# Performance work log

Hardware: AMD Instinct MI355X
Metric: run time of the kernel (lower is better)

Reference implementation:

```python
import jax, jax.numpy as jnp
import numpy as np

N_NODES = 50000
N_EDGES = 800000
IN_DIM = 1280
HID = 512
EMB = 64
LN_EPS = 1e-5
NEG_SLOPE = 0.2  # DGL GATConv default leaky_relu slope


def setup_inputs() -> dict:
    key = jax.random.key(0)
    ks = jax.random.split(key, 10)
    features = jax.random.normal(ks[0], (N_NODES, IN_DIM), dtype=jnp.float32)
    src = jax.random.randint(ks[1], (N_EDGES,), 0, N_NODES)
    dst = jax.random.randint(ks[2], (N_EDGES,), 0, N_NODES)
    # MLPBlock params: Linear(IN_DIM -> HID) + LayerNorm(HID)
    W1 = jax.random.normal(ks[3], (IN_DIM, HID), dtype=jnp.float32) / np.sqrt(IN_DIM)
    b1 = jnp.zeros((HID,), dtype=jnp.float32)
    ln_g = jnp.ones((HID,), dtype=jnp.float32)
    ln_b = jnp.zeros((HID,), dtype=jnp.float32)
    # GATConv params (num_heads=1): fc (no bias), attn_l, attn_r, output bias
    Wg = jax.random.normal(ks[4], (HID, EMB), dtype=jnp.float32) / np.sqrt(HID)
    attn_l = jax.random.normal(ks[5], (EMB,), dtype=jnp.float32) * 0.1
    attn_r = jax.random.normal(ks[6], (EMB,), dtype=jnp.float32) * 0.1
    bias_g = jnp.zeros((EMB,), dtype=jnp.float32)
    return {"features": features, "src": src, "dst": dst, "W1": W1, "b1": b1,
            "ln_g": ln_g, "ln_b": ln_b, "Wg": Wg, "attn_l": attn_l,
            "attn_r": attn_r, "bias_g": bias_g}


def reference(features, src, dst, W1, b1, ln_g, ln_b, Wg, attn_l, attn_r, bias_g):
    # MLPBlock: linear -> ReLU -> LayerNorm (dropout is identity in eval)
    x = jax.nn.relu(features @ W1 + b1)                     # [N, HID]
    mu = jnp.mean(x, axis=-1, keepdims=True)
    var = jnp.mean(jnp.square(x - mu), axis=-1, keepdims=True)
    x = (x - mu) * jax.lax.rsqrt(var + LN_EPS) * ln_g + ln_b

    # GATConv (single head)
    feat = x @ Wg                                           # [N, EMB]
    el = feat @ attn_l                                      # [N]
    er = feat @ attn_r                                      # [N]
    e = jax.nn.leaky_relu(el[src] + er[dst], NEG_SLOPE)     # [E]

    # edge softmax over incoming edges of each dst node
    m = jax.ops.segment_max(e, dst, num_segments=N_NODES)   # [N]
    ex = jnp.exp(e - m[dst])                                # [E]
    s = jax.ops.segment_sum(ex, dst, num_segments=N_NODES)  # [N]
    a = ex / s[dst]                                         # [E]

    # scatter-aggregate weighted source features
    out = jax.ops.segment_sum(a[:, None] * feat[src], dst, num_segments=N_NODES)
    return out + bias_g                                     # [N, EMB] (head dim squeezed)
```

## Files before the change

### kernel.cpp

```cpp
#include <hip/hip_runtime.h>
#include <hip/hip_bf16.h>
#include <stdint.h>

#define N_NODES 50000
#define N_EDGES 800000
#define IN_DIM 1280
#define HID 512
#define EMB 64
#define M_PAD 50048
#define MT1 391
#define LN_EPS 1e-5f

typedef __attribute__((ext_vector_type(8))) __bf16 bf16x8;
typedef __attribute__((ext_vector_type(4))) float floatx4;

#define AS1C(p) ((const __attribute__((address_space(1))) void*)(p))
#define AS3(p)  ((__attribute__((address_space(3))) void*)(p))

__device__ __forceinline__ unsigned f2bf(float f) {
  unsigned u = __float_as_uint(f);
  u += 0x7FFFu + ((u >> 16) & 1u);
  return u >> 16;
}
__device__ __forceinline__ float bf2f(unsigned short s) {
  return __uint_as_float(((unsigned)s) << 16);
}

__global__ __launch_bounds__(256) void k_prep(const float* __restrict__ W1,
                                              const float* __restrict__ Wg,
                                              unsigned short* __restrict__ B1t,
                                              unsigned short* __restrict__ Wgt,
                                              int* __restrict__ deg) {
  int idx = blockIdx.x * 256 + threadIdx.x;
  if (idx < HID * IN_DIM) {
    int n = idx / IN_DIM;
    int k = idx - n * IN_DIM;
    B1t[idx] = (unsigned short)f2bf(W1[(size_t)k * HID + n]);
  }
  if (idx < EMB * HID) {
    int n = idx >> 9;
    int k = idx & 511;
    Wgt[idx] = (unsigned short)f2bf(Wg[(size_t)k * EMB + n]);
  }
  if (idx < N_NODES) deg[idx] = 0;
}

__global__ __launch_bounds__(256) void k_conv(const float* __restrict__ F,
                                              unsigned short* __restrict__ Fb) {
  size_t base = ((size_t)blockIdx.x * 256 + threadIdx.x) * 8;
  uint4 o;
  if (base < (size_t)N_NODES * IN_DIM) {
    float4 f0 = *(const float4*)(F + base);
    float4 f1 = *(const float4*)(F + base + 4);
    o.x = f2bf(f0.x) | (f2bf(f0.y) << 16);
    o.y = f2bf(f0.z) | (f2bf(f0.w) << 16);
    o.z = f2bf(f1.x) | (f2bf(f1.y) << 16);
    o.w = f2bf(f1.z) | (f2bf(f1.w) << 16);
  } else {
    o = make_uint4(0u, 0u, 0u, 0u);
  }
  *(uint4*)(Fb + base) = o;
}

__device__ __forceinline__ int swz(int r) { return (r ^ (r >> 2)) & 3; }

__global__ __launch_bounds__(256) void k_gemm1(const unsigned short* __restrict__ Abf,
                                               const unsigned short* __restrict__ Bt,
                                               const float* __restrict__ bias1,
                                               unsigned short* __restrict__ xn) {
  __shared__ unsigned short As[128 * 32];
  __shared__ unsigned short Bs[128 * 32];
  const int t = threadIdx.x;
  const int bm = blockIdx.x, bn = blockIdx.y;
  const int w = t >> 6, lane = t & 63, quad = lane >> 4, lr = lane & 15;
  const int wm = (w & 1) * 64, wn = (w >> 1) * 64;

  floatx4 acc[4][4];
#pragma unroll
  for (int i = 0; i < 4; ++i)
#pragma unroll
    for (int j = 0; j < 4; ++j) acc[i][j] = (floatx4){0.f, 0.f, 0.f, 0.f};

  const int r0 = t >> 2, c0 = (t & 3) ^ swz(t >> 2);
  const int r1 = 64 + (t >> 2), c1 = (t & 3) ^ swz(64 + (t >> 2));
  const unsigned short* a0 = Abf + (size_t)(bm * 128 + r0) * IN_DIM + c0 * 8;
  const unsigned short* a1 = Abf + (size_t)(bm * 128 + r1) * IN_DIM + c1 * 8;
  const unsigned short* b0 = Bt + (size_t)(bn * 128 + r0) * IN_DIM + c0 * 8;
  const unsigned short* b1 = Bt + (size_t)(bn * 128 + r1) * IN_DIM + c1 * 8;
  unsigned short* asw = As + w * 512;
  unsigned short* bsw = Bs + w * 512;

  const int q2 = quad ^ swz(lr);

  for (int k0 = 0; k0 < IN_DIM; k0 += 32) {
    __builtin_amdgcn_global_load_lds(AS1C(a0 + k0), AS3(asw), 16, 0, 0);
    __builtin_amdgcn_global_load_lds(AS1C(a1 + k0), AS3(asw + 2048), 16, 0, 0);
    __builtin_amdgcn_global_load_lds(AS1C(b0 + k0), AS3(bsw), 16, 0, 0);
    __builtin_amdgcn_global_load_lds(AS1C(b1 + k0), AS3(bsw + 2048), 16, 0, 0);
    __syncthreads();

    bf16x8 af[4], bfv[4];
#pragma unroll
    for (int mi = 0; mi < 4; ++mi)
      af[mi] = *(const bf16x8*)&As[(wm + mi * 16 + lr) * 32 + q2 * 8];
#pragma unroll
    for (int ni = 0; ni < 4; ++ni)
      bfv[ni] = *(const bf16x8*)&Bs[(wn + ni * 16 + lr) * 32 + q2 * 8];
#pragma unroll
    for (int mi = 0; mi < 4; ++mi)
#pragma unroll
      for (int ni = 0; ni < 4; ++ni)
        acc[mi][ni] = __builtin_amdgcn_mfma_f32_16x16x32_bf16(af[mi], bfv[ni], acc[mi][ni], 0, 0, 0);
    __syncthreads();
  }

#pragma unroll
  for (int mi = 0; mi < 4; ++mi) {
    int gr = bm * 128 + wm + mi * 16 + quad * 4;
#pragma unroll
    for (int ni = 0; ni < 4; ++ni) {
      int gc = bn * 128 + wn + ni * 16 + lr;
      float bv = bias1[gc];
#pragma unroll
      for (int r = 0; r < 4; ++r) {
        float v = acc[mi][ni][r] + bv;
        v = v > 0.f ? v : 0.f;
        xn[(size_t)(gr + r) * HID + gc] = (unsigned short)f2bf(v);
      }
    }
  }
}

__global__ __launch_bounds__(256) void k_ln(unsigned short* __restrict__ xn,
                                            const float* __restrict__ g,
                                            const float* __restrict__ b) {
  int w = threadIdx.x >> 6, lane = threadIdx.x & 63;
  int row = blockIdx.x * 4 + w;
  unsigned short* p = xn + (size_t)row * HID + lane * 8;
  uint4 raw = *(const uint4*)p;
  float x[8];
  x[0] = bf2f((unsigned short)(raw.x & 0xFFFF)); x[1] = bf2f((unsigned short)(raw.x >> 16));
  x[2] = bf2f((unsigned short)(raw.y & 0xFFFF)); x[3] = bf2f((unsigned short)(raw.y >> 16));
  x[4] = bf2f((unsigned short)(raw.z & 0xFFFF)); x[5] = bf2f((unsigned short)(raw.z >> 16));
  x[6] = bf2f((unsigned short)(raw.w & 0xFFFF)); x[7] = bf2f((unsigned short)(raw.w >> 16));
  float s1 = 0.f, s2 = 0.f;
#pragma unroll
  for (int j = 0; j < 8; ++j) { s1 += x[j]; s2 += x[j] * x[j]; }
#pragma unroll
  for (int m = 1; m < 64; m <<= 1) {
    s1 += __shfl_xor(s1, m, 64);
    s2 += __shfl_xor(s2, m, 64);
  }
  float mu = s1 * (1.f / HID);
  float var = s2 * (1.f / HID) - mu * mu;
  float rs = rsqrtf(var + LN_EPS);
  const float* gp = g + lane * 8;
  const float* bp = b + lane * 8;
  float4 g0 = *(const float4*)gp, g1 = *(const float4*)(gp + 4);
  float4 b0 = *(const float4*)bp, b1v = *(const float4*)(bp + 4);
  float y0 = (x[0] - mu) * rs * g0.x + b0.x;
  float y1 = (x[1] - mu) * rs * g0.y + b0.y;
  float y2 = (x[2] - mu) * rs * g0.z + b0.z;
  float y3 = (x[3] - mu) * rs * g0.w + b0.w;
  float y4 = (x[4] - mu) * rs * g1.x + b1v.x;
  float y5 = (x[5] - mu) * rs * g1.y + b1v.y;
  float y6 = (x[6] - mu) * rs * g1.z + b1v.z;
  float y7 = (x[7] - mu) * rs * g1.w + b1v.w;
  uint4 o;
  o.x = f2bf(y0) | (f2bf(y1) << 16);
  o.y = f2bf(y2) | (f2bf(y3) << 16);
  o.z = f2bf(y4) | (f2bf(y5) << 16);
  o.w = f2bf(y6) | (f2bf(y7) << 16);
  *(uint4*)p = o;
}

__global__ __launch_bounds__(256) void k_gemm2(const unsigned short* __restrict__ Xn,
                                               const unsigned short* __restrict__ Wgt,
                                               const float* __restrict__ al,
                                               const float* __restrict__ ar,
                                               float* __restrict__ feat,
                                               float* __restrict__ el,
                                               float* __restrict__ er) {
  __shared__ unsigned short As[128 * 32];
  __shared__ unsigned short Bs[64 * 32];
  const int t = threadIdx.x;
  const int bm = blockIdx.x;
  const int w = t >> 6, lane = t & 63, quad = lane >> 4, lr = lane & 15;

  floatx4 acc[2][4];
#pragma unroll
  for (int i = 0; i < 2; ++i)
#pragma unroll
    for (int j = 0; j < 4; ++j) acc[i][j] = (floatx4){0.f, 0.f, 0.f, 0.f};

  const int r0 = t >> 2, c0 = (t & 3) ^ swz(t >> 2);
  const int r1 = 64 + (t >> 2), c1 = (t & 3) ^ swz(64 + (t >> 2));
  const unsigned short* a0 = Xn + (size_t)(bm * 128 + r0) * HID + c0 * 8;
  const unsigned short* a1 = Xn + (size_t)(bm * 128 + r1) * HID + c1 * 8;
  const unsigned short* b0 = Wgt + (size_t)r0 * HID + c0 * 8;
  unsigned short* asw = As + w * 512;
  unsigned short* bsw = Bs + w * 512;

  const int q2 = quad ^ swz(lr);

  for (int k0 = 0; k0 < HID; k0 += 32) {
    __builtin_amdgcn_global_load_lds(AS1C(a0 + k0), AS3(asw), 16, 0, 0);
    __builtin_amdgcn_global_load_lds(AS1C(a1 + k0), AS3(asw + 2048), 16, 0, 0);
    __builtin_amdgcn_global_load_lds(AS1C(b0 + k0), AS3(bsw), 16, 0, 0);
    __syncthreads();

    bf16x8 af[2], bfv[4];
#pragma unroll
    for (int mi = 0; mi < 2; ++mi)
      af[mi] = *(const bf16x8*)&As[(w * 32 + mi * 16 + lr) * 32 + q2 * 8];
#pragma unroll
    for (int ni = 0; ni < 4; ++ni)
      bfv[ni] = *(const bf16x8*)&Bs[(ni * 16 + lr) * 32 + q2 * 8];
#pragma unroll
    for (int mi = 0; mi < 2; ++mi)
#pragma unroll
      for (int ni = 0; ni < 4; ++ni)
        acc[mi][ni] = __builtin_amdgcn_mfma_f32_16x16x32_bf16(af[mi], bfv[ni], acc[mi][ni], 0, 0, 0);
    __syncthreads();
  }

  float alv[4], arv[4];
#pragma unroll
  for (int ni = 0; ni < 4; ++ni) {
    alv[ni] = al[ni * 16 + lr];
    arv[ni] = ar[ni * 16 + lr];
  }
#pragma unroll
  for (int mi = 0; mi < 2; ++mi) {
    int gr = bm * 128 + w * 32 + mi * 16 + quad * 4;
#pragma unroll
    for (int r = 0; r < 4; ++r) {
      float sl = 0.f, sr2 = 0.f;
#pragma unroll
      for (int ni = 0; ni < 4; ++ni) {
        float v = acc[mi][ni][r];
        feat[(size_t)(gr + r) * EMB + ni * 16 + lr] = v;
        sl += v * alv[ni];
        sr2 += v * arv[ni];
      }
#pragma unroll
      for (int m = 1; m < 16; m <<= 1) {
        sl += __shfl_xor(sl, m, 64);
        sr2 += __shfl_xor(sr2, m, 64);
      }
      if (lr == 0) {
        el[gr + r] = sl;
        er[gr + r] = sr2;
      }
    }
  }
}

__global__ __launch_bounds__(256) void k_hist(const int* __restrict__ dst,
                                              int* __restrict__ deg) {
  int t = blockIdx.x * 256 + threadIdx.x;
  if (t < N_EDGES) atomicAdd(&deg[dst[t]], 1);
}

__global__ __launch_bounds__(256) void k_scan1(const int* __restrict__ deg,
                                               int* __restrict__ rowstart,
                                               int* __restrict__ bsum) {
  __shared__ int sh[256];
  int t = threadIdx.x, i = blockIdx.x * 256 + t;
  int x = (i < N_NODES) ? deg[i] : 0;
  sh[t] = x;
  __syncthreads();
  for (int off = 1; off < 256; off <<= 1) {
    int v = (t >= off) ? sh[t - off] : 0;
    __syncthreads();
    sh[t] += v;
    __syncthreads();
  }
  if (i < N_NODES) rowstart[i] = sh[t] - x;
  if (t == 255) bsum[blockIdx.x] = sh[255];
}

__global__ __launch_bounds__(256) void k_scan2(const int* __restrict__ bsum,
                                               int* __restrict__ boff) {
  __shared__ int sh[256];
  int t = threadIdx.x;
  int x = (t < 196) ? bsum[t] : 0;
  sh[t] = x;
  __syncthreads();
  for (int off = 1; off < 256; off <<= 1) {
    int v = (t >= off) ? sh[t - off] : 0;
    __syncthreads();
    sh[t] += v;
    __syncthreads();
  }
  boff[t] = sh[t] - x;
}

__global__ __launch_bounds__(256) void k_scan3(int* __restrict__ rowstart,
                                               const int* __restrict__ boff,
                                               int* __restrict__ cursor) {
  int i = blockIdx.x * 256 + threadIdx.x;
  if (i < N_NODES) {
    int rs = rowstart[i] + boff[i >> 8];
    rowstart[i] = rs;
    cursor[i] = rs;
  }
}

__global__ __launch_bounds__(256) void k_fill(const int* __restrict__ src,
                                              const int* __restrict__ dst,
                                              int* __restrict__ cursor,
                                              int* __restrict__ csr_src) {
  int t = blockIdx.x * 256 + threadIdx.x;
  if (t >= N_EDGES) return;
  int pos = atomicAdd(&cursor[dst[t]], 1);
  csr_src[pos] = src[t];
}

__global__ __launch_bounds__(256) void k_gat(const int* __restrict__ rowstart,
                                             const int* __restrict__ deg,
                                             const int* __restrict__ csr_src,
                                             const float* __restrict__ el,
                                             const float* __restrict__ er,
                                             const float* __restrict__ feat,
                                             const float* __restrict__ bias_g,
                                             float* __restrict__ out) {
  int w = threadIdx.x >> 6, lane = threadIdx.x & 63;
  int v = blockIdx.x * 4 + w;
  int start = rowstart[v], d = deg[v];
  float erv = er[v];
  float m = -3.4e38f, s = 0.f, O = 0.f;
  for (int i = 0; i < d; ++i) {
    int sv = csr_src[start + i];
    float f = feat[(size_t)sv * EMB + lane];
    float e = el[sv] + erv;
    e = e > 0.f ? e : 0.2f * e;
    if (e <= m) {
      float p = __expf(e - m);
      s += p;
      O = fmaf(p, f, O);
    } else {
      float a = __expf(m - e);
      s = fmaf(s, a, 1.f);
      O = fmaf(O, a, f);
      m = e;
    }
  }
  out[(size_t)v * EMB + lane] = (d > 0 ? O / s : 0.f) + bias_g[lane];
}

extern "C" void kernel_launch(void* const* d_in, const int* in_sizes, int n_in,
                              void* d_out, int out_size, void* d_ws, size_t ws_size,
                              hipStream_t stream) {
  const float* features = (const float*)d_in[0];
  const int* src        = (const int*)d_in[1];
  const int* dst        = (const int*)d_in[2];
  const float* W1       = (const float*)d_in[3];
  const float* b1       = (const float*)d_in[4];
  const float* ln_g     = (const float*)d_in[5];
  const float* ln_b     = (const float*)d_in[6];
  const float* Wg       = (const float*)d_in[7];
  const float* attn_l   = (const float*)d_in[8];
  const float* attn_r   = (const float*)d_in[9];
  const float* bias_g   = (const float*)d_in[10];
  float* out = (float*)d_out;

  char* ws = (char*)d_ws;
  size_t off = 0;
  auto alloc = [&](size_t bytes) {
    char* p = ws + off;
    off = (off + bytes + 255) & ~(size_t)255;
    return p;
  };
  unsigned short* B1t   = (unsigned short*)alloc((size_t)HID * IN_DIM * 2);
  unsigned short* Wgt   = (unsigned short*)alloc((size_t)EMB * HID * 2);
  unsigned short* featbf= (unsigned short*)alloc((size_t)M_PAD * IN_DIM * 2);
  unsigned short* xn    = (unsigned short*)alloc((size_t)M_PAD * HID * 2);
  float* feat           = (float*)alloc((size_t)M_PAD * EMB * 4);
  float* el             = (float*)alloc((size_t)M_PAD * 4);
  float* er             = (float*)alloc((size_t)M_PAD * 4);
  int* deg              = (int*)alloc((size_t)N_NODES * 4);
  int* rowstart         = (int*)alloc((size_t)N_NODES * 4);
  int* cursor           = (int*)alloc((size_t)N_NODES * 4);
  int* bsum             = (int*)alloc(256 * 4);
  int* boff             = (int*)alloc(256 * 4);
  int* csr_src          = (int*)alloc((size_t)N_EDGES * 4);
  (void)ws_size; (void)in_sizes; (void)n_in; (void)out_size;

  k_prep<<<dim3(2560), dim3(256), 0, stream>>>(W1, Wg, B1t, Wgt, deg);
  k_conv<<<dim3(31280), dim3(256), 0, stream>>>(features, featbf);
  k_hist<<<dim3(3125), dim3(256), 0, stream>>>(dst, deg);
  k_scan1<<<dim3(196), dim3(256), 0, stream>>>(deg, rowstart, bsum);
  k_scan2<<<dim3(1), dim3(256), 0, stream>>>(bsum, boff);
  k_scan3<<<dim3(196), dim3(256), 0, stream>>>(rowstart, boff, cursor);
  k_fill<<<dim3(3125), dim3(256), 0, stream>>>(src, dst, cursor, csr_src);
  k_gemm1<<<dim3(MT1, 4), dim3(256), 0, stream>>>(featbf, B1t, b1, xn);
  k_ln<<<dim3(M_PAD / 4), dim3(256), 0, stream>>>(xn, ln_g, ln_b);
  k_gemm2<<<dim3(MT1), dim3(256), 0, stream>>>(xn, Wgt, attn_l, attn_r, feat, el, er);
  k_gat<<<dim3(12500), dim3(256), 0, stream>>>(rowstart, deg, csr_src, el, er, feat, bias_g, out);
}
```

Measured before the change: 701.9 us.

## Fold LayerNorm into GEMM epilogues, fuse conv/hist and scans, widen GEMM1 K-tile

```diff
diff --git a/kernel.cpp b/kernel.cpp
--- a/kernel.cpp
+++ b/kernel.cpp
@@ -28,9 +28,15 @@
 
 __global__ __launch_bounds__(256) void k_prep(const float* __restrict__ W1,
                                               const float* __restrict__ Wg,
+                                              const float* __restrict__ ln_g,
+                                              const float* __restrict__ ln_b,
                                               unsigned short* __restrict__ B1t,
-                                              unsigned short* __restrict__ Wgt,
-                                              int* __restrict__ deg) {
+                                              unsigned short* __restrict__ Wgp,
+                                              float* __restrict__ uvec,
+                                              float* __restrict__ vvec,
+                                              int* __restrict__ deg,
+                                              float* __restrict__ s1,
+                                              float* __restrict__ s2) {
   int idx = blockIdx.x * 256 + threadIdx.x;
   if (idx < HID * IN_DIM) {
     int n = idx / IN_DIM;
@@ -40,36 +46,54 @@
   if (idx < EMB * HID) {
     int n = idx >> 9;
     int k = idx & 511;
-    Wgt[idx] = (unsigned short)f2bf(Wg[(size_t)k * EMB + n]);
+    Wgp[idx] = (unsigned short)f2bf(ln_g[k] * Wg[(size_t)k * EMB + n]);
+  }
+  if (idx < EMB) {
+    float su = 0.f, sv = 0.f;
+    for (int k = 0; k < HID; ++k) {
+      float wv = Wg[(size_t)k * EMB + idx];
+      su += ln_b[k] * wv;
+      sv += ln_g[k] * wv;
+    }
+    uvec[idx] = su;
+    vvec[idx] = sv;
   }
   if (idx < N_NODES) deg[idx] = 0;
-}
-
-__global__ __launch_bounds__(256) void k_conv(const float* __restrict__ F,
-                                              unsigned short* __restrict__ Fb) {
-  size_t base = ((size_t)blockIdx.x * 256 + threadIdx.x) * 8;
-  uint4 o;
-  if (base < (size_t)N_NODES * IN_DIM) {
-    float4 f0 = *(const float4*)(F + base);
-    float4 f1 = *(const float4*)(F + base + 4);
-    o.x = f2bf(f0.x) | (f2bf(f0.y) << 16);
-    o.y = f2bf(f0.z) | (f2bf(f0.w) << 16);
-    o.z = f2bf(f1.x) | (f2bf(f1.y) << 16);
-    o.w = f2bf(f1.z) | (f2bf(f1.w) << 16);
+  if (idx < M_PAD) { s1[idx] = 0.f; s2[idx] = 0.f; }
+}
+
+__global__ __launch_bounds__(256) void k_convhist(const float* __restrict__ F,
+                                                  unsigned short* __restrict__ Fb,
+                                                  const int* __restrict__ dst,
+                                                  int* __restrict__ deg) {
+  if (blockIdx.x < 31280) {
+    size_t base = ((size_t)blockIdx.x * 256 + threadIdx.x) * 8;
+    uint4 o;
+    if (base < (size_t)N_NODES * IN_DIM) {
+      float4 f0 = *(const float4*)(F + base);
+      float4 f1 = *(const float4*)(F + base + 4);
+      o.x = f2bf(f0.x) | (f2bf(f0.y) << 16);
+      o.y = f2bf(f0.z) | (f2bf(f0.w) << 16);
+      o.z = f2bf(f1.x) | (f2bf(f1.y) << 16);
+      o.w = f2bf(f1.z) | (f2bf(f1.w) << 16);
+    } else {
+      o = make_uint4(0u, 0u, 0u, 0u);
+    }
+    *(uint4*)(Fb + base) = o;
   } else {
-    o = make_uint4(0u, 0u, 0u, 0u);
-  }
-  *(uint4*)(Fb + base) = o;
-}
-
-__device__ __forceinline__ int swz(int r) { return (r ^ (r >> 2)) & 3; }
+    int t = (blockIdx.x - 31280) * 256 + threadIdx.x;
+    if (t < N_EDGES) atomicAdd(&deg[dst[t]], 1);
+  }
+}
 
 __global__ __launch_bounds__(256) void k_gemm1(const unsigned short* __restrict__ Abf,
                                                const unsigned short* __restrict__ Bt,
                                                const float* __restrict__ bias1,
-                                               unsigned short* __restrict__ xn) {
-  __shared__ unsigned short As[128 * 32];
-  __shared__ unsigned short Bs[128 * 32];
+                                               unsigned short* __restrict__ xn,
+                                               float* __restrict__ s1,
+                                               float* __restrict__ s2) {
+  __shared__ unsigned short As[128 * 64];
+  __shared__ unsigned short Bs[128 * 64];
   const int t = threadIdx.x;
   const int bm = blockIdx.x, bn = blockIdx.y;
   const int w = t >> 6, lane = t & 63, quad = lane >> 4, lr = lane & 15;
@@ -81,36 +105,44 @@
 #pragma unroll
     for (int j = 0; j < 4; ++j) acc[i][j] = (floatx4){0.f, 0.f, 0.f, 0.f};
 
-  const int r0 = t >> 2, c0 = (t & 3) ^ swz(t >> 2);
-  const int r1 = 64 + (t >> 2), c1 = (t & 3) ^ swz(64 + (t >> 2));
-  const unsigned short* a0 = Abf + (size_t)(bm * 128 + r0) * IN_DIM + c0 * 8;
-  const unsigned short* a1 = Abf + (size_t)(bm * 128 + r1) * IN_DIM + c1 * 8;
-  const unsigned short* b0 = Bt + (size_t)(bn * 128 + r0) * IN_DIM + c0 * 8;
-  const unsigned short* b1 = Bt + (size_t)(bn * 128 + r1) * IN_DIM + c1 * 8;
+  const int rr = t >> 3;
+  const int cc = (t & 7) ^ (rr & 7);
+  const unsigned short* aP[4];
+  const unsigned short* bP[4];
+#pragma unroll
+  for (int j = 0; j < 4; ++j) {
+    aP[j] = Abf + (size_t)(bm * 128 + j * 32 + rr) * IN_DIM + cc * 8;
+    bP[j] = Bt + (size_t)(bn * 128 + j * 32 + rr) * IN_DIM + cc * 8;
+  }
   unsigned short* asw = As + w * 512;
   unsigned short* bsw = Bs + w * 512;
 
-  const int q2 = quad ^ swz(lr);
-
-  for (int k0 = 0; k0 < IN_DIM; k0 += 32) {
-    __builtin_amdgcn_global_load_lds(AS1C(a0 + k0), AS3(asw), 16, 0, 0);
-    __builtin_amdgcn_global_load_lds(AS1C(a1 + k0), AS3(asw + 2048), 16, 0, 0);
-    __builtin_amdgcn_global_load_lds(AS1C(b0 + k0), AS3(bsw), 16, 0, 0);
-    __builtin_amdgcn_global_load_lds(AS1C(b1 + k0), AS3(bsw + 2048), 16, 0, 0);
-    __syncthreads();
-
-    bf16x8 af[4], bfv[4];
-#pragma unroll
-    for (int mi = 0; mi < 4; ++mi)
-      af[mi] = *(const bf16x8*)&As[(wm + mi * 16 + lr) * 32 + q2 * 8];
-#pragma unroll
-    for (int ni = 0; ni < 4; ++ni)
-      bfv[ni] = *(const bf16x8*)&Bs[(wn + ni * 16 + lr) * 32 + q2 * 8];
-#pragma unroll
-    for (int mi = 0; mi < 4; ++mi)
+  const int l7 = lr & 7;
+
+  for (int k0 = 0; k0 < IN_DIM; k0 += 64) {
+#pragma unroll
+    for (int j = 0; j < 4; ++j) {
+      __builtin_amdgcn_global_load_lds(AS1C(aP[j] + k0), AS3(asw + j * 2048), 16, 0, 0);
+      __builtin_amdgcn_global_load_lds(AS1C(bP[j] + k0), AS3(bsw + j * 2048), 16, 0, 0);
+    }
+    __syncthreads();
+
+#pragma unroll
+    for (int h = 0; h < 2; ++h) {
+      const int col = ((h * 4 + quad) ^ l7) * 8;
+      bf16x8 af[4], bfv[4];
+#pragma unroll
+      for (int mi = 0; mi < 4; ++mi)
+        af[mi] = *(const bf16x8*)&As[(wm + mi * 16 + lr) * 64 + col];
 #pragma unroll
       for (int ni = 0; ni < 4; ++ni)
-        acc[mi][ni] = __builtin_amdgcn_mfma_f32_16x16x32_bf16(af[mi], bfv[ni], acc[mi][ni], 0, 0, 0);
+        bfv[ni] = *(const bf16x8*)&Bs[(wn + ni * 16 + lr) * 64 + col];
+#pragma unroll
+      for (int mi = 0; mi < 4; ++mi)
+#pragma unroll
+        for (int ni = 0; ni < 4; ++ni)
+          acc[mi][ni] = __builtin_amdgcn_mfma_f32_16x16x32_bf16(af[mi], bfv[ni], acc[mi][ni], 0, 0, 0);
+    }
     __syncthreads();
   }
 
@@ -118,64 +150,40 @@
   for (int mi = 0; mi < 4; ++mi) {
     int gr = bm * 128 + wm + mi * 16 + quad * 4;
 #pragma unroll
-    for (int ni = 0; ni < 4; ++ni) {
-      int gc = bn * 128 + wn + ni * 16 + lr;
-      float bv = bias1[gc];
-#pragma unroll
-      for (int r = 0; r < 4; ++r) {
-        float v = acc[mi][ni][r] + bv;
+    for (int r = 0; r < 4; ++r) {
+      float ps1 = 0.f, ps2 = 0.f;
+#pragma unroll
+      for (int ni = 0; ni < 4; ++ni) {
+        int gc = bn * 128 + wn + ni * 16 + lr;
+        float v = acc[mi][ni][r] + bias1[gc];
         v = v > 0.f ? v : 0.f;
-        xn[(size_t)(gr + r) * HID + gc] = (unsigned short)f2bf(v);
-      }
-    }
-  }
-}
-
-__global__ __launch_bounds__(256) void k_ln(unsigned short* __restrict__ xn,
-                                            const float* __restrict__ g,
-                                            const float* __restrict__ b) {
-  int w = threadIdx.x >> 6, lane = threadIdx.x & 63;
-  int row = blockIdx.x * 4 + w;
-  unsigned short* p = xn + (size_t)row * HID + lane * 8;
-  uint4 raw = *(const uint4*)p;
-  float x[8];
-  x[0] = bf2f((unsigned short)(raw.x & 0xFFFF)); x[1] = bf2f((unsigned short)(raw.x >> 16));
-  x[2] = bf2f((unsigned short)(raw.y & 0xFFFF)); x[3] = bf2f((unsigned short)(raw.y >> 16));
-  x[4] = bf2f((unsigned short)(raw.z & 0xFFFF)); x[5] = bf2f((unsigned short)(raw.z >> 16));
-  x[6] = bf2f((unsigned short)(raw.w & 0xFFFF)); x[7] = bf2f((unsigned short)(raw.w >> 16));
-  float s1 = 0.f, s2 = 0.f;
-#pragma unroll
-  for (int j = 0; j < 8; ++j) { s1 += x[j]; s2 += x[j] * x[j]; }
-#pragma unroll
-  for (int m = 1; m < 64; m <<= 1) {
-    s1 += __shfl_xor(s1, m, 64);
-    s2 += __shfl_xor(s2, m, 64);
-  }
-  float mu = s1 * (1.f / HID);
-  float var = s2 * (1.f / HID) - mu * mu;
-  float rs = rsqrtf(var + LN_EPS);
-  const float* gp = g + lane * 8;
-  const float* bp = b + lane * 8;
-  float4 g0 = *(const float4*)gp, g1 = *(const float4*)(gp + 4);
-  float4 b0 = *(const float4*)bp, b1v = *(const float4*)(bp + 4);
-  float y0 = (x[0] - mu) * rs * g0.x + b0.x;
-  float y1 = (x[1] - mu) * rs * g0.y + b0.y;
-  float y2 = (x[2] - mu) * rs * g0.z + b0.z;
-  float y3 = (x[3] - mu) * rs * g0.w + b0.w;
-  float y4 = (x[4] - mu) * rs * g1.x + b1v.x;
-  float y5 = (x[5] - mu) * rs * g1.y + b1v.y;
-  float y6 = (x[6] - mu) * rs * g1.z + b1v.z;
-  float y7 = (x[7] - mu) * rs * g1.w + b1v.w;
-  uint4 o;
-  o.x = f2bf(y0) | (f2bf(y1) << 16);
-  o.y = f2bf(y2) | (f2bf(y3) << 16);
-  o.z = f2bf(y4) | (f2bf(y5) << 16);
-  o.w = f2bf(y6) | (f2bf(y7) << 16);
-  *(uint4*)p = o;
-}
+        unsigned short h = (unsigned short)f2bf(v);
+        xn[(size_t)(gr + r) * HID + gc] = h;
+        float vr = bf2f(h);
+        ps1 += vr;
+        ps2 += vr * vr;
+      }
+#pragma unroll
+      for (int m = 1; m < 16; m <<= 1) {
+        ps1 += __shfl_xor(ps1, m, 64);
+        ps2 += __shfl_xor(ps2, m, 64);
+      }
+      if (lr == 0) {
+        atomicAdd(&s1[gr + r], ps1);
+        atomicAdd(&s2[gr + r], ps2);
+      }
+    }
+  }
+}
+
+__device__ __forceinline__ int swz(int r) { return (r ^ (r >> 2)) & 3; }
 
 __global__ __launch_bounds__(256) void k_gemm2(const unsigned short* __restrict__ Xn,
-                                               const unsigned short* __restrict__ Wgt,
+                                               const unsigned short* __restrict__ Wgp,
+                                               const float* __restrict__ s1,
+                                               const float* __restrict__ s2,
+                                               const float* __restrict__ uvec,
+                                               const float* __restrict__ vvec,
                                                const float* __restrict__ al,
                                                const float* __restrict__ ar,
                                                float* __restrict__ feat,
@@ -197,7 +205,7 @@
   const int r1 = 64 + (t >> 2), c1 = (t & 3) ^ swz(64 + (t >> 2));
   const unsigned short* a0 = Xn + (size_t)(bm * 128 + r0) * HID + c0 * 8;
   const unsigned short* a1 = Xn + (size_t)(bm * 128 + r1) * HID + c1 * 8;
-  const unsigned short* b0 = Wgt + (size_t)r0 * HID + c0 * 8;
+  const unsigned short* b0 = Wgp + (size_t)r0 * HID + c0 * 8;
   unsigned short* asw = As + w * 512;
   unsigned short* bsw = Bs + w * 512;
 
@@ -224,22 +232,28 @@
     __syncthreads();
   }
 
-  float alv[4], arv[4];
+  float alv[4], arv[4], uv[4], vv[4];
 #pragma unroll
   for (int ni = 0; ni < 4; ++ni) {
     alv[ni] = al[ni * 16 + lr];
     arv[ni] = ar[ni * 16 + lr];
+    uv[ni] = uvec[ni * 16 + lr];
+    vv[ni] = vvec[ni * 16 + lr];
   }
 #pragma unroll
   for (int mi = 0; mi < 2; ++mi) {
     int gr = bm * 128 + w * 32 + mi * 16 + quad * 4;
 #pragma unroll
     for (int r = 0; r < 4; ++r) {
+      int row = gr + r;
+      float mu = s1[row] * (1.f / HID);
+      float rs = rsqrtf(s2[row] * (1.f / HID) - mu * mu + LN_EPS);
+      float mrs = mu * rs;
       float sl = 0.f, sr2 = 0.f;
 #pragma unroll
       for (int ni = 0; ni < 4; ++ni) {
-        float v = acc[mi][ni][r];
-        feat[(size_t)(gr + r) * EMB + ni * 16 + lr] = v;
+        float v = rs * acc[mi][ni][r] + uv[ni] - mrs * vv[ni];
+        feat[(size_t)row * EMB + ni * 16 + lr] = v;
         sl += v * alv[ni];
         sr2 += v * arv[ni];
       }
@@ -249,17 +263,11 @@
         sr2 += __shfl_xor(sr2, m, 64);
       }
       if (lr == 0) {
-        el[gr + r] = sl;
-        er[gr + r] = sr2;
-      }
-    }
-  }
-}
-
-__global__ __launch_bounds__(256) void k_hist(const int* __restrict__ dst,
-                                              int* __restrict__ deg) {
-  int t = blockIdx.x * 256 + threadIdx.x;
-  if (t < N_EDGES) atomicAdd(&deg[dst[t]], 1);
+        el[row] = sl;
+        er[row] = sr2;
+      }
+    }
+  }
 }
 
 __global__ __launch_bounds__(256) void k_scan1(const int* __restrict__ deg,
@@ -280,8 +288,9 @@
   if (t == 255) bsum[blockIdx.x] = sh[255];
 }
 
-__global__ __launch_bounds__(256) void k_scan2(const int* __restrict__ bsum,
-                                               int* __restrict__ boff) {
+__global__ __launch_bounds__(256) void k_scan23(const int* __restrict__ bsum,
+                                                int* __restrict__ rowstart,
+                                                int* __restrict__ cursor) {
   __shared__ int sh[256];
   int t = threadIdx.x;
   int x = (t < 196) ? bsum[t] : 0;
@@ -293,15 +302,11 @@
     sh[t] += v;
     __syncthreads();
   }
-  boff[t] = sh[t] - x;
-}
-
-__global__ __launch_bounds__(256) void k_scan3(int* __restrict__ rowstart,
-                                               const int* __restrict__ boff,
-                                               int* __restrict__ cursor) {
-  int i = blockIdx.x * 256 + threadIdx.x;
+  int boff = (blockIdx.x > 0) ? sh[blockIdx.x - 1] : 0;
+  __syncthreads();
+  int i = blockIdx.x * 256 + t;
   if (i < N_NODES) {
-    int rs = rowstart[i] + boff[i >> 8];
+    int rs = rowstart[i] + boff;
     rowstart[i] = rs;
     cursor[i] = rs;
   }
@@ -329,22 +334,16 @@
   int v = blockIdx.x * 4 + w;
   int start = rowstart[v], d = deg[v];
   float erv = er[v];
-  float m = -3.4e38f, s = 0.f, O = 0.f;
+  float s = 0.f, O = 0.f;
+#pragma unroll 4
   for (int i = 0; i < d; ++i) {
     int sv = csr_src[start + i];
     float f = feat[(size_t)sv * EMB + lane];
     float e = el[sv] + erv;
     e = e > 0.f ? e : 0.2f * e;
-    if (e <= m) {
-      float p = __expf(e - m);
-      s += p;
-      O = fmaf(p, f, O);
-    } else {
-      float a = __expf(m - e);
-      s = fmaf(s, a, 1.f);
-      O = fmaf(O, a, f);
-      m = e;
-    }
+    float p = __expf(e);
+    s += p;
+    O = fmaf(p, f, O);
   }
   out[(size_t)v * EMB + lane] = (d > 0 ? O / s : 0.f) + bias_g[lane];
 }
@@ -373,29 +372,31 @@
     return p;
   };
   unsigned short* B1t   = (unsigned short*)alloc((size_t)HID * IN_DIM * 2);
-  unsigned short* Wgt   = (unsigned short*)alloc((size_t)EMB * HID * 2);
+  unsigned short* Wgp   = (unsigned short*)alloc((size_t)EMB * HID * 2);
   unsigned short* featbf= (unsigned short*)alloc((size_t)M_PAD * IN_DIM * 2);
   unsigned short* xn    = (unsigned short*)alloc((size_t)M_PAD * HID * 2);
   float* feat           = (float*)alloc((size_t)M_PAD * EMB * 4);
   float* el             = (float*)alloc((size_t)M_PAD * 4);
   float* er             = (float*)alloc((size_t)M_PAD * 4);
+  float* s1             = (float*)alloc((size_t)M_PAD * 4);
+  float* s2             = (float*)alloc((size_t)M_PAD * 4);
+  float* uvec           = (float*)alloc(EMB * 4);
+  float* vvec           = (float*)alloc(EMB * 4);
   int* deg              = (int*)alloc((size_t)N_NODES * 4);
   int* rowstart         = (int*)alloc((size_t)N_NODES * 4);
   int* cursor           = (int*)alloc((size_t)N_NODES * 4);
   int* bsum             = (int*)alloc(256 * 4);
-  int* boff             = (int*)alloc(256 * 4);
   int* csr_src          = (int*)alloc((size_t)N_EDGES * 4);
   (void)ws_size; (void)in_sizes; (void)n_in; (void)out_size;
 
-  k_prep<<<dim3(2560), dim3(256), 0, stream>>>(W1, Wg, B1t, Wgt, deg);
-  k_conv<<<dim3(31280), dim3(256), 0, stream>>>(features, featbf);
-  k_hist<<<dim3(3125), dim3(256), 0, stream>>>(dst, deg);
+  k_prep<<<dim3(2560), dim3(256), 0, stream>>>(W1, Wg, ln_g, ln_b, B1t, Wgp,
+                                               uvec, vvec, deg, s1, s2);
+  k_convhist<<<dim3(31280 + 3125), dim3(256), 0, stream>>>(features, featbf, dst, deg);
   k_scan1<<<dim3(196), dim3(256), 0, stream>>>(deg, rowstart, bsum);
-  k_scan2<<<dim3(1), dim3(256), 0, stream>>>(bsum, boff);
-  k_scan3<<<dim3(196), dim3(256), 0, stream>>>(rowstart, boff, cursor);
+  k_scan23<<<dim3(196), dim3(256), 0, stream>>>(bsum, rowstart, cursor);
   k_fill<<<dim3(3125), dim3(256), 0, stream>>>(src, dst, cursor, csr_src);
-  k_gemm1<<<dim3(MT1, 4), dim3(256), 0, stream>>>(featbf, B1t, b1, xn);
-  k_ln<<<dim3(M_PAD / 4), dim3(256), 0, stream>>>(xn, ln_g, ln_b);
-  k_gemm2<<<dim3(MT1), dim3(256), 0, stream>>>(xn, Wgt, attn_l, attn_r, feat, el, er);
+  k_gemm1<<<dim3(MT1, 4), dim3(256), 0, stream>>>(featbf, B1t, b1, xn, s1, s2);
+  k_gemm2<<<dim3(MT1), dim3(256), 0, stream>>>(xn, Wgp, s1, s2, uvec, vvec,
+                                               attn_l, attn_r, feat, el, er);
   k_gat<<<dim3(12500), dim3(256), 0, stream>>>(rowstart, deg, csr_src, el, er, feat, bias_g, out);
 }
```

Measured after the change: 674.1 us. 1.04x faster.
